# Performance work log

Measured on AMD Instinct MI355X. Metric: run time of the kernel, lower is better.

## Reference

```python
import jax, jax.numpy as jnp
import numpy as np

IN_F, HID_F, OUT_F = 2048, 8192, 2048
BATCH = 4096

def setup_inputs() -> dict:
    key = jax.random.key(0)
    k_x, k_w1, k_b1, k_w2, k_b2 = jax.random.split(key, 5)
    # PyTorch Linear default init: U(-1/sqrt(fan_in), 1/sqrt(fan_in))
    s1 = 1.0 / np.sqrt(IN_F)
    s2 = 1.0 / np.sqrt(HID_F)
    return {
        "x":  jax.random.normal(k_x, (BATCH, IN_F), dtype=jnp.float32),
        "W1": jax.random.uniform(k_w1, (IN_F, HID_F), jnp.float32, -s1, s1),
        "b1": jax.random.uniform(k_b1, (HID_F,), jnp.float32, -s1, s1),
        "W2": jax.random.uniform(k_w2, (HID_F, OUT_F), jnp.float32, -s2, s2),
        "b2": jax.random.uniform(k_b2, (OUT_F,), jnp.float32, -s2, s2),
    }

def reference(x, W1, b1, W2, b2):
    # linear1 -> ReLU -> linear2 -> sigmoid (the original's numpy "black box"
    # is mathematically 1/(1+exp(-x)), done here on-device).
    h = jax.nn.relu(x @ W1 + b1)          # [B, hidden]
    z = h @ W2 + b2                        # [B, out]
    return jax.nn.sigmoid(z)
```

## Files before the change

### kernel.cpp

```cpp
#include <hip/hip_runtime.h>
#include <hip/hip_bf16.h>
#include <stdint.h>

#define IN_F  2048
#define HID_F 8192
#define OUT_F 2048
#define BATCH 4096

typedef __attribute__((ext_vector_type(8))) short bf16x8;
typedef __attribute__((ext_vector_type(4))) float f32x4;

__device__ __forceinline__ unsigned short f32_to_bf16(float f) {
  union { float f; uint32_t u; } v; v.f = f;
  uint32_t u = v.u;
  uint32_t r = u + 0x7FFF + ((u >> 16) & 1);
  return (unsigned short)(r >> 16);
}

__device__ __forceinline__ void load_lds16(const unsigned short* g, unsigned short* l) {
  __builtin_amdgcn_global_load_lds(
      (const __attribute__((address_space(1))) void*)g,
      (__attribute__((address_space(3))) void*)l, 16, 0, 0);
}


__global__ void cvt_f32_bf16(const float* __restrict__ in, unsigned short* __restrict__ out, int n4) {
  int i = blockIdx.x * blockDim.x + threadIdx.x;
  int stride = gridDim.x * blockDim.x;
  for (int idx = i; idx < n4; idx += stride) {
    float4 v = ((const float4*)in)[idx];
    ushort4 o;
    o.x = f32_to_bf16(v.x); o.y = f32_to_bf16(v.y);
    o.z = f32_to_bf16(v.z); o.w = f32_to_bf16(v.w);
    ((ushort4*)out)[idx] = o;
  }
}

__global__ void transpose_cvt(const float* __restrict__ in, unsigned short* __restrict__ out,
                              int R, int C) {
  __shared__ float tile[32][33];
  const int tx = threadIdx.x;
  const int ty = threadIdx.y;
  const int c0 = blockIdx.x * 32;
  const int r0 = blockIdx.y * 32;
  #pragma unroll
  for (int i = ty; i < 32; i += 8)
    tile[i][tx] = in[(size_t)(r0 + i) * C + c0 + tx];
  __syncthreads();
  #pragma unroll
  for (int i = ty; i < 32; i += 8)
    out[(size_t)(c0 + i) * R + r0 + tx] = f32_to_bf16(tile[tx][i]);
}

template <int EPI>
__global__ __launch_bounds__(256, 2)
void gemm_bt(const unsigned short* __restrict__ A, const unsigned short* __restrict__ Bt,
             const float* __restrict__ bias, void* __restrict__ C,
             int M, int N, int K) {
  __shared__ unsigned short lA[128 * 64];
  __shared__ unsigned short lB[128 * 64];

  const int tid  = threadIdx.x;
  const int lane = tid & 63;
  const int wave = tid >> 6;
  const int wr = wave >> 1;
  const int wc = wave & 1;

  const int nbx  = N >> 7;
  const int brow = blockIdx.x / nbx;
  const int bcol = blockIdx.x % nbx;

  f32x4 acc[4][4] = {};

  const int ar   = tid >> 3;
  const int acol = (tid & 7) * 8;
  const unsigned short* Ag = A  + (size_t)(brow * 128 + ar) * K + acol;
  const unsigned short* Bg = Bt + (size_t)(bcol * 128 + ar) * K + acol;
  unsigned short* lAp = lA + tid * 8;
  unsigned short* lBp = lB + tid * 8;

  const int fr = lane & 15;
  const int fk = (lane >> 4) * 8;

  for (int kt = 0; kt < K; kt += 64) {
    __syncthreads();
    #pragma unroll
    for (int c = 0; c < 4; ++c) {
      load_lds16(Ag + (size_t)(c * 32) * K + kt, lAp + c * 2048);
      load_lds16(Bg + (size_t)(c * 32) * K + kt, lBp + c * 2048);
    }
    __syncthreads();
    #pragma unroll
    for (int kk = 0; kk < 2; ++kk) {
      bf16x8 af[4], bf[4];
      #pragma unroll
      for (int m = 0; m < 4; ++m)
        af[m] = *(const bf16x8*)&lA[(wr * 64 + m * 16 + fr) * 64 + kk * 32 + fk];
      #pragma unroll
      for (int n = 0; n < 4; ++n)
        bf[n] = *(const bf16x8*)&lB[(wc * 64 + n * 16 + fr) * 64 + kk * 32 + fk];
      #pragma unroll
      for (int m = 0; m < 4; ++m)
        #pragma unroll
        for (int n = 0; n < 4; ++n)
          acc[m][n] = __builtin_amdgcn_mfma_f32_16x16x32_bf16(af[m], bf[n], acc[m][n], 0, 0, 0);
    }
  }

  const int crow0 = brow * 128 + wr * 64 + (lane >> 4) * 4;
  const int ccol0 = bcol * 128 + wc * 64 + (lane & 15);
  #pragma unroll
  for (int n = 0; n < 4; ++n) {
    const int col = ccol0 + n * 16;
    const float bv = bias[col];
    #pragma unroll
    for (int m = 0; m < 4; ++m) {
      #pragma unroll
      for (int i = 0; i < 4; ++i) {
        const size_t idx = (size_t)(crow0 + m * 16 + i) * N + col;
        float v = acc[m][n][i] + bv;
        if (EPI == 0) {
          v = v > 0.f ? v : 0.f;
          ((unsigned short*)C)[idx] = f32_to_bf16(v);
        } else {
          ((float*)C)[idx] = 1.f / (1.f + __expf(-v));
        }
      }
    }
  }
}


extern "C" void kernel_launch(void* const* d_in, const int* in_sizes, int n_in,
                              void* d_out, int out_size, void* d_ws, size_t ws_size,
                              hipStream_t stream) {
  const float* x  = (const float*)d_in[0];
  const float* W1 = (const float*)d_in[1];
  const float* b1 = (const float*)d_in[2];
  const float* W2 = (const float*)d_in[3];
  const float* b2 = (const float*)d_in[4];
  float* out = (float*)d_out;

  char* ws = (char*)d_ws;
  const size_t MB = 1024 * 1024;
  unsigned short* x_bf = (unsigned short*)(ws);
  unsigned short* W1t  = (unsigned short*)(ws + 16 * MB);
  unsigned short* W2t  = (unsigned short*)(ws + 48 * MB);
  unsigned short* h_bf = (unsigned short*)(ws + 80 * MB);

  cvt_f32_bf16<<<2048, 256, 0, stream>>>(x, x_bf, (BATCH * IN_F) / 4);
  transpose_cvt<<<dim3(HID_F / 32, IN_F / 32), dim3(32, 8), 0, stream>>>(W1, W1t, IN_F, HID_F);
  transpose_cvt<<<dim3(OUT_F / 32, HID_F / 32), dim3(32, 8), 0, stream>>>(W2, W2t, HID_F, OUT_F);

  gemm_bt<0><<<(BATCH / 128) * (HID_F / 128), 256, 0, stream>>>(
      x_bf, W1t, b1, h_bf, BATCH, HID_F, IN_F);
  gemm_bt<1><<<(BATCH / 128) * (OUT_F / 128), 256, 0, stream>>>(
      h_bf, W2t, b2, out, BATCH, OUT_F, HID_F);
}
```

Before: 522.0 us.

## Triple-buffer GEMM with swizzled LDS, larger tiles, XCD remap, vectorized transpose

The GEMM moves to 512 threads with a 128x256 block tile. It keeps a three-slot LDS ring fed by async global-to-LDS loads so the next tiles are prefetched while MFMAs run, replacing the load-sync-compute loop. LDS addresses are XOR-swizzled to avoid bank conflicts, workgroups are remapped across XCDs, and s_setprio is raised around the MFMA block. The transpose kernel now uses 64x64 tiles with float4 reads and 16-byte bf16 writes. The larger LDS footprint (144KB) limits occupancy, and the hand-placed waitcnt and barriers are fragile.

```diff
diff --git a/kernel.cpp b/kernel.cpp
--- a/kernel.cpp
+++ b/kernel.cpp
@@ -9,6 +9,7 @@
 
 typedef __attribute__((ext_vector_type(8))) short bf16x8;
 typedef __attribute__((ext_vector_type(4))) float f32x4;
+typedef __attribute__((ext_vector_type(8))) unsigned short u16x8;
 
 __device__ __forceinline__ unsigned short f32_to_bf16(float f) {
   union { float f; uint32_t u; } v; v.f = f;
@@ -17,7 +18,7 @@
   return (unsigned short)(r >> 16);
 }
 
-__device__ __forceinline__ void load_lds16(const unsigned short* g, unsigned short* l) {
+__device__ __forceinline__ void stage16(const unsigned short* g, unsigned short* l) {
   __builtin_amdgcn_global_load_lds(
       (const __attribute__((address_space(1))) void*)g,
       (__attribute__((address_space(3))) void*)l, 16, 0, 0);
@@ -38,77 +39,147 @@
 
 __global__ void transpose_cvt(const float* __restrict__ in, unsigned short* __restrict__ out,
                               int R, int C) {
-  __shared__ float tile[32][33];
-  const int tx = threadIdx.x;
-  const int ty = threadIdx.y;
-  const int c0 = blockIdx.x * 32;
-  const int r0 = blockIdx.y * 32;
-  #pragma unroll
-  for (int i = ty; i < 32; i += 8)
-    tile[i][tx] = in[(size_t)(r0 + i) * C + c0 + tx];
+  __shared__ unsigned short t[64][72];
+  const int tid = threadIdx.x;
+  const int r0 = blockIdx.y * 64;
+  const int c0 = blockIdx.x * 64;
+  #pragma unroll
+  for (int p = 0; p < 4; ++p) {
+    int f4  = p * 256 + tid;
+    int row = f4 >> 4;
+    int c   = (f4 & 15) * 4;
+    float4 v = *(const float4*)&in[(size_t)(r0 + row) * C + c0 + c];
+    t[c + 0][row] = f32_to_bf16(v.x);
+    t[c + 1][row] = f32_to_bf16(v.y);
+    t[c + 2][row] = f32_to_bf16(v.z);
+    t[c + 3][row] = f32_to_bf16(v.w);
+  }
   __syncthreads();
   #pragma unroll
-  for (int i = ty; i < 32; i += 8)
-    out[(size_t)(c0 + i) * R + r0 + tx] = f32_to_bf16(tile[tx][i]);
+  for (int p = 0; p < 2; ++p) {
+    int u  = p * 256 + tid;
+    int cc = u >> 3;
+    int rr = (u & 7) * 8;
+    *(u16x8*)&out[(size_t)(c0 + cc) * R + r0 + rr] = *(const u16x8*)&t[cc][rr];
+  }
 }
 
 template <int EPI>
-__global__ __launch_bounds__(256, 2)
+__global__ __launch_bounds__(512, 2)
 void gemm_bt(const unsigned short* __restrict__ A, const unsigned short* __restrict__ Bt,
              const float* __restrict__ bias, void* __restrict__ C,
              int M, int N, int K) {
-  __shared__ unsigned short lA[128 * 64];
-  __shared__ unsigned short lB[128 * 64];
+  __shared__ unsigned short lA[3][128 * 64];
+  __shared__ unsigned short lB[3][256 * 64];
 
   const int tid  = threadIdx.x;
   const int lane = tid & 63;
   const int wave = tid >> 6;
-  const int wr = wave >> 1;
-  const int wc = wave & 1;
-
-  const int nbx  = N >> 7;
-  const int brow = blockIdx.x / nbx;
-  const int bcol = blockIdx.x % nbx;
+  const int wr = wave >> 2;
+  const int wc = wave & 3;
+
+  const int nbx = N >> 8;
+  const int nwg = (M >> 7) * nbx;
+  int wg = blockIdx.x;
+  wg = (wg & 7) * (nwg >> 3) + (wg >> 3);
+  const int brow = wg / nbx;
+  const int bcol = wg % nbx;
+
+  const int srow = tid >> 3;
+  const int w8   = (tid & 7) * 8;
+  const unsigned short* gA[2];
+  const unsigned short* gB[4];
+  #pragma unroll
+  for (int c = 0; c < 2; ++c) {
+    int row = c * 64 + srow;
+    gA[c] = A + (size_t)(brow * 128 + row) * K + (w8 ^ ((row & 7) << 3));
+  }
+  #pragma unroll
+  for (int c = 0; c < 4; ++c) {
+    int row = c * 64 + srow;
+    gB[c] = Bt + (size_t)(bcol * 256 + row) * K + (w8 ^ ((row & 7) << 3));
+  }
+  const int ldst = tid * 8;
+
+  const int ktiles = K >> 6;
+
+  #pragma unroll
+  for (int c = 0; c < 2; ++c) stage16(gA[c],      &lA[0][c * 4096 + ldst]);
+  #pragma unroll
+  for (int c = 0; c < 4; ++c) stage16(gB[c],      &lB[0][c * 4096 + ldst]);
+  #pragma unroll
+  for (int c = 0; c < 2; ++c) stage16(gA[c] + 64, &lA[1][c * 4096 + ldst]);
+  #pragma unroll
+  for (int c = 0; c < 4; ++c) stage16(gB[c] + 64, &lB[1][c * 4096 + ldst]);
+  #pragma unroll
+  for (int c = 0; c < 2; ++c) gA[c] += 128;
+  #pragma unroll
+  for (int c = 0; c < 4; ++c) gB[c] += 128;
+
+  asm volatile("s_waitcnt vmcnt(6)" ::: "memory");
+  __builtin_amdgcn_s_barrier();
 
   f32x4 acc[4][4] = {};
-
-  const int ar   = tid >> 3;
-  const int acol = (tid & 7) * 8;
-  const unsigned short* Ag = A  + (size_t)(brow * 128 + ar) * K + acol;
-  const unsigned short* Bg = Bt + (size_t)(bcol * 128 + ar) * K + acol;
-  unsigned short* lAp = lA + tid * 8;
-  unsigned short* lBp = lB + tid * 8;
-
   const int fr = lane & 15;
   const int fk = (lane >> 4) * 8;
 
-  for (int kt = 0; kt < K; kt += 64) {
-    __syncthreads();
-    #pragma unroll
-    for (int c = 0; c < 4; ++c) {
-      load_lds16(Ag + (size_t)(c * 32) * K + kt, lAp + c * 2048);
-      load_lds16(Bg + (size_t)(c * 32) * K + kt, lBp + c * 2048);
-    }
-    __syncthreads();
+  int slot = 0;
+  for (int jt = 0; jt < ktiles; ++jt) {
+    const int nslot = (slot + 2 >= 3) ? slot - 1 : slot + 2;
+    const bool pf = (jt + 2 < ktiles);
+
     #pragma unroll
     for (int kk = 0; kk < 2; ++kk) {
       bf16x8 af[4], bf[4];
       #pragma unroll
-      for (int m = 0; m < 4; ++m)
-        af[m] = *(const bf16x8*)&lA[(wr * 64 + m * 16 + fr) * 64 + kk * 32 + fk];
-      #pragma unroll
-      for (int n = 0; n < 4; ++n)
-        bf[n] = *(const bf16x8*)&lB[(wc * 64 + n * 16 + fr) * 64 + kk * 32 + fk];
+      for (int m = 0; m < 4; ++m) {
+        int row = wr * 64 + m * 16 + fr;
+        af[m] = *(const bf16x8*)&lA[slot][row * 64 + ((kk * 32 + fk) ^ ((row & 7) << 3))];
+      }
+      #pragma unroll
+      for (int n = 0; n < 4; ++n) {
+        int row = wc * 64 + n * 16 + fr;
+        bf[n] = *(const bf16x8*)&lB[slot][row * 64 + ((kk * 32 + fk) ^ ((row & 7) << 3))];
+      }
+      if (pf) {
+        if (kk == 0) {
+          stage16(gA[0], &lA[nslot][0 * 4096 + ldst]);
+          stage16(gA[1], &lA[nslot][1 * 4096 + ldst]);
+          stage16(gB[0], &lB[nslot][0 * 4096 + ldst]);
+        } else {
+          stage16(gB[1], &lB[nslot][1 * 4096 + ldst]);
+          stage16(gB[2], &lB[nslot][2 * 4096 + ldst]);
+          stage16(gB[3], &lB[nslot][3 * 4096 + ldst]);
+        }
+      }
+      __builtin_amdgcn_s_barrier();
+      asm volatile("s_waitcnt lgkmcnt(0)" ::: "memory");
+      __builtin_amdgcn_s_setprio(1);
       #pragma unroll
       for (int m = 0; m < 4; ++m)
         #pragma unroll
         for (int n = 0; n < 4; ++n)
           acc[m][n] = __builtin_amdgcn_mfma_f32_16x16x32_bf16(af[m], bf[n], acc[m][n], 0, 0, 0);
-    }
+      __builtin_amdgcn_s_setprio(0);
+      __builtin_amdgcn_s_barrier();
+    }
+
+    if (pf) {
+      #pragma unroll
+      for (int c = 0; c < 2; ++c) gA[c] += 64;
+      #pragma unroll
+      for (int c = 0; c < 4; ++c) gB[c] += 64;
+    }
+    if (jt + 1 < ktiles) {
+      if (pf) asm volatile("s_waitcnt vmcnt(6)" ::: "memory");
+      else    asm volatile("s_waitcnt vmcnt(0)" ::: "memory");
+      __builtin_amdgcn_s_barrier();
+    }
+    slot = (slot + 1 >= 3) ? 0 : slot + 1;
   }
 
   const int crow0 = brow * 128 + wr * 64 + (lane >> 4) * 4;
-  const int ccol0 = bcol * 128 + wc * 64 + (lane & 15);
+  const int ccol0 = bcol * 256 + wc * 64 + fr;
   #pragma unroll
   for (int n = 0; n < 4; ++n) {
     const int col = ccol0 + n * 16;
@@ -149,11 +220,11 @@
   unsigned short* h_bf = (unsigned short*)(ws + 80 * MB);
 
   cvt_f32_bf16<<<2048, 256, 0, stream>>>(x, x_bf, (BATCH * IN_F) / 4);
-  transpose_cvt<<<dim3(HID_F / 32, IN_F / 32), dim3(32, 8), 0, stream>>>(W1, W1t, IN_F, HID_F);
-  transpose_cvt<<<dim3(OUT_F / 32, HID_F / 32), dim3(32, 8), 0, stream>>>(W2, W2t, HID_F, OUT_F);
-
-  gemm_bt<0><<<(BATCH / 128) * (HID_F / 128), 256, 0, stream>>>(
+  transpose_cvt<<<dim3(HID_F / 64, IN_F / 64), 256, 0, stream>>>(W1, W1t, IN_F, HID_F);
+  transpose_cvt<<<dim3(OUT_F / 64, HID_F / 64), 256, 0, stream>>>(W2, W2t, HID_F, OUT_F);
+
+  gemm_bt<0><<<(BATCH / 128) * (HID_F / 256), 512, 0, stream>>>(
       x_bf, W1t, b1, h_bf, BATCH, HID_F, IN_F);
-  gemm_bt<1><<<(BATCH / 128) * (OUT_F / 128), 256, 0, stream>>>(
+  gemm_bt<1><<<(BATCH / 128) * (OUT_F / 256), 512, 0, stream>>>(
       h_bf, W2t, b2, out, BATCH, OUT_F, HID_F);
 }
```

Measured after the change: 511.0 us. -2.1%, faster.
